# Kernel tuning notes

Measured on AMD Instinct MI355X. Metric: run time of the kernel, lower is better.

## Reference

```python
import jax, jax.numpy as jnp
import numpy as np

C = 180; NH = 6; WS = 8; SS = 4; MLP_RATIO = 2
HD = C // NH
SCALE = HD ** (-0.5)
N = WS * WS  # tokens per window


def _rel_pos_index():
    coords = np.stack(np.meshgrid(np.arange(WS), np.arange(WS), indexing='ij'))  # (2,WS,WS)
    flat = coords.reshape(2, -1)  # (2, N)
    rel = (flat[:, :, None] - flat[:, None, :]).transpose(1, 2, 0)  # (N,N,2)
    rel = rel + np.array([WS - 1, WS - 1])
    rel[:, :, 0] *= 2 * WS - 1
    return rel.sum(-1)  # (N,N) int


def _shift_mask(H, W):
    img_mask = np.zeros((H, W), dtype=np.float32)
    slices = (slice(0, -WS), slice(-WS, -SS), slice(-SS, None))
    cnt = 0
    for hs in slices:
        for ws_ in slices:
            img_mask[hs, ws_] = cnt
            cnt += 1
    mw = img_mask.reshape(H // WS, WS, W // WS, WS).transpose(0, 2, 1, 3).reshape(-1, N)  # (nW, N)
    am = mw[:, None, :] - mw[:, :, None]  # (nW, N, N)
    return np.where(am != 0, np.float32(-100.0), np.float32(0.0))


def _partition(x, H, W):
    # (B,H,W,C) -> (B*nW, N, C)
    B = x.shape[0]
    x = x.reshape(B, H // WS, WS, W // WS, WS, C).transpose(0, 1, 3, 2, 4, 5)
    return x.reshape(-1, N, C)


def _combine(w, B, H, W):
    # (B*nW, N, C) -> (B,H,W,C)
    x = w.reshape(B, H // WS, W // WS, WS, WS, C).transpose(0, 1, 3, 2, 4, 5)
    return x.reshape(B, H, W, C)


def _ln(x, g, b):
    mu = jnp.mean(x, -1, keepdims=True)
    var = jnp.mean(jnp.square(x - mu), -1, keepdims=True)
    return (x - mu) * jax.lax.rsqrt(var + 1e-5) * g + b


def setup_inputs() -> dict:
    key = jax.random.key(0)
    ks = jax.random.split(key, 10)
    B, H, W = 16, 128, 128
    s = 0.02
    return {
        'x': jax.random.normal(ks[0], (B, H * W, C), jnp.float32),
        'ln1_g': jnp.ones((C,), jnp.float32), 'ln1_b': jnp.zeros((C,), jnp.float32),
        'qkv_w': jax.random.normal(ks[1], (3 * C, C), jnp.float32) * s,
        'qkv_b': jnp.zeros((3 * C,), jnp.float32),
        'proj_w': jax.random.normal(ks[2], (C, C), jnp.float32) * s,
        'proj_b': jnp.zeros((C,), jnp.float32),
        'rpb_table': jax.random.normal(ks[3], ((2 * WS - 1) ** 2, NH), jnp.float32) * s,
        'ln2_g': jnp.ones((C,), jnp.float32), 'ln2_b': jnp.zeros((C,), jnp.float32),
        'fc1_w': jax.random.normal(ks[4], (MLP_RATIO * C, C), jnp.float32) * s,
        'fc1_b': jnp.zeros((MLP_RATIO * C,), jnp.float32),
        'fc2_w': jax.random.normal(ks[5], (C, MLP_RATIO * C), jnp.float32) * s,
        'fc2_b': jnp.zeros((C,), jnp.float32),
        'img_height': 128, 'img_width': 128,
    }


def reference(x, ln1_g, ln1_b, qkv_w, qkv_b, proj_w, proj_b, rpb_table,
              ln2_g, ln2_b, fc1_w, fc1_b, fc2_w, fc2_b, img_height, img_width):
    H, W = int(img_height), int(img_width)
    B = x.shape[0]
    rpi = jnp.asarray(_rel_pos_index().reshape(-1))           # (N*N,) static
    mask = jnp.asarray(_shift_mask(H, W))                     # (nW, N, N) static
    nW = (H // WS) * (W // WS)

    residual = x
    h = _ln(x, ln1_g, ln1_b).reshape(B, H, W, C)
    h = jnp.roll(h, (-SS, -SS), axis=(1, 2))
    xw = _partition(h, H, W)                                  # (B*nW, N, C)

    qkv = xw @ qkv_w.T + qkv_b                                # (B*nW, N, 3C)
    qkv = qkv.reshape(-1, N, 3, NH, HD).transpose(2, 0, 3, 1, 4)
    q, k, v = qkv[0] * SCALE, qkv[1], qkv[2]                  # (B*nW, NH, N, HD)
    scores = jnp.einsum('whnd,whmd->whnm', q, k)              # (B*nW, NH, N, N)
    bias = rpb_table[rpi].reshape(N, N, NH).transpose(2, 0, 1)  # (NH,N,N)
    scores = scores + bias[None]
    scores = scores.reshape(B, nW, NH, N, N) + mask[None, :, None]
    probs = jax.nn.softmax(scores.reshape(-1, NH, N, N), axis=-1)
    out = jnp.einsum('whnm,whmd->whnd', probs, v)             # (B*nW, NH, N, HD)
    out = out.transpose(0, 2, 1, 3).reshape(-1, N, C)
    out = out @ proj_w.T + proj_b

    h = _combine(out, B, H, W)
    h = jnp.roll(h, (SS, SS), axis=(1, 2)).reshape(B, H * W, C)
    h = h + residual
    m = _ln(h, ln2_g, ln2_b)
    m = jax.nn.gelu(m @ fc1_w.T + fc1_b, approximate=False) @ fc2_w.T + fc2_b
    return h + m
```

## Files before the change

kernel.cpp:

```cpp
#include <hip/hip_runtime.h>
#include <hip/hip_bf16.h>

typedef short s16x8 __attribute__((ext_vector_type(8)));
typedef short s16x4 __attribute__((ext_vector_type(4)));
typedef float f32x4 __attribute__((ext_vector_type(4)));

__device__ __forceinline__ short f2bf(float f) {
    __bf16 h = (__bf16)f;
    return __builtin_bit_cast(short, h);
}
__device__ __forceinline__ float bf2f(short s) {
    return __builtin_bit_cast(float, ((unsigned int)(unsigned short)s) << 16);
}
__device__ __forceinline__ unsigned int pk2(float a, float b) {
    return (unsigned int)(unsigned short)f2bf(a) | ((unsigned int)(unsigned short)f2bf(b) << 16);
}
__device__ __forceinline__ float plo(unsigned int u) { return bf2f((short)(u & 0xFFFFu)); }
__device__ __forceinline__ float phi(unsigned int u) { return bf2f((short)(u >> 16)); }
__device__ __forceinline__ f32x4 mfma16(s16x8 a, s16x8 b, f32x4 c) {
    return __builtin_amdgcn_mfma_f32_16x16x32_bf16(a, b, c, 0, 0, 0);
}
__device__ __forceinline__ s16x8 ld_b64x2(const short* p) {
    union { s16x8 v; s16x4 h[2]; } u;
    u.h[0] = *(const s16x4*)p;
    u.h[1] = *(const s16x4*)(p + 4);
    return u.v;
}
__device__ __forceinline__ s16x4 pack4(f32x4 a) {
    s16x4 w;
    w[0] = f2bf(a[0]); w[1] = f2bf(a[1]); w[2] = f2bf(a[2]); w[3] = f2bf(a[3]);
    return w;
}

#define SCALE_Q 0.18257418583505536f
#define ONE_BF16 ((short)0x3F80)
#define RA 204
#define PS 76
#define HS 108


__global__ void k_prep(const float* __restrict__ qkv_w, const float* __restrict__ qkv_b,
                       const float* __restrict__ proj_w, const float* __restrict__ proj_b,
                       const float* __restrict__ fc1_w, const float* __restrict__ fc1_b,
                       const float* __restrict__ fc2_w,
                       const float* __restrict__ rpb,
                       short* __restrict__ Whead, short* __restrict__ Wproj,
                       short* __restrict__ Wfc1, short* __restrict__ Wfc2,
                       short* __restrict__ battn) {
    int gt = blockIdx.x * 256 + threadIdx.x;
    int stride = gridDim.x * 256;
    for (int idx = gt; idx < 6 * 96 * 192; idx += stride) {
        int h = idx / (96 * 192), rem = idx - h * 96 * 192;
        int rr = rem / 192, kk = rem - rr * 192;
        int seg = rr >> 5, hd = rr & 31;
        float val = 0.f;
        if (hd < 30) {
            int ch = seg * 180 + h * 30 + hd;
            if (kk < 180) val = qkv_w[ch * 180 + kk];
            else if (kk == 180) val = qkv_b[ch];
            if (seg == 0) val *= SCALE_Q;
        }
        Whead[idx] = f2bf(val);
    }
    for (int idx = gt; idx < 192 * 192; idx += stride) {
        int rr = idx / 192, kk = idx - rr * 192;
        float val = 0.f;
        if (rr < 180) {
            if (kk < 180) val = proj_w[rr * 180 + kk];
            else if (kk == 180) val = proj_b[rr];
        }
        Wproj[idx] = f2bf(val);
    }
    for (int idx = gt; idx < 384 * 192; idx += stride) {
        int rr = idx / 192, kk = idx - rr * 192;
        float val = 0.f;
        if (rr < 360) {
            if (kk < 180) val = fc1_w[rr * 180 + kk];
            else if (kk == 180) val = fc1_b[rr];
        }
        Wfc1[idx] = f2bf(val);
    }
    for (int idx = gt; idx < 192 * 384; idx += stride) {
        int rr = idx / 384, kk = idx - rr * 384;
        Wfc2[idx] = (rr < 180 && kk < 360) ? f2bf(fc2_w[rr * 360 + kk]) : (short)0;
    }
    for (int idx = gt; idx < 6 * 64 * 64; idx += stride) {
        int h = idx >> 12, n = (idx >> 6) & 63, m = idx & 63;
        int r1 = n >> 3, c1 = n & 7, r2 = m >> 3, c2 = m & 7;
        int ridx = (r1 - r2 + 7) * 15 + (c1 - c2 + 7);
        battn[idx] = f2bf(rpb[ridx * 6 + h]);
    }
}

__global__ __launch_bounds__(768, 3)
void k_fused(const float* __restrict__ x, const float* __restrict__ g1, const float* __restrict__ b1,
             const short* __restrict__ Whead,
             const short* __restrict__ Wproj,
             const short* __restrict__ battn,
             const float* __restrict__ g2, const float* __restrict__ b2,
             const short* __restrict__ Wfc1,
             const short* __restrict__ Wfc2, const float* __restrict__ fb2,
             float* __restrict__ out) {
    __shared__ __align__(16) char smem[138240];

    const int tid = threadIdx.x;
    const int wvg = tid >> 6;
    const int half = (wvg >= 6) ? 1 : 0;
    const int wv = wvg - half * 6;
    const int l = tid & 63, l15 = l & 15, lg = l >> 4;
    const int tl = tid - half * 384;

    char* sm = smem + half * 69120;
    short* xln  = (short*)sm;
    short* xout = (short*)sm;
    short* ylds = (short*)sm;
    short* mo   = (short*)sm;
    short* regP = (short*)(sm + 26112);
    short* pout = regP;
    short* ybuf = regP;
    short* hid  = (short*)(sm + 55296);
    short* patch = regP + wv * 2432;

    const int wid = blockIdx.x * 2 + half;
    const int b = wid >> 8, win = wid & 255, wi = win >> 4, wj = win & 15;
    const bool edge = (wi == 15) || (wj == 15);
    const f32x4 vzero = {0.f, 0.f, 0.f, 0.f};

    const int t = tl >> 2, sub = tl & 3;
    size_t rowbase = 0;
    if (tl < 256) {
        const int r = t >> 3, c = t & 7;
        const int gi = (wi * 8 + r + 4) & 127, gj = (wj * 8 + c + 4) & 127;
        rowbase = ((size_t)b * 16384 + (size_t)gi * 128 + gj) * 180;
    }
    const float* xrow = x + rowbase;
    float* yrow = out + rowbase;

    if (tl < 256) {
        float s1 = 0.f, s2 = 0.f;
        unsigned int pA[12], pB[12];
#pragma unroll
        for (int m = 0; m < 12; ++m) {
            int jj = sub + 4 * m;
            if (jj < 45) {
                float4 t4 = *(const float4*)&xrow[4 * jj];
                s1 += t4.x + t4.y + t4.z + t4.w;
                s2 += t4.x * t4.x + t4.y * t4.y + t4.z * t4.z + t4.w * t4.w;
                pA[m] = pk2(t4.x, t4.y);
                pB[m] = pk2(t4.z, t4.w);
            }
        }
        s1 += __shfl_xor(s1, 1); s2 += __shfl_xor(s2, 1);
        s1 += __shfl_xor(s1, 2); s2 += __shfl_xor(s2, 2);
        const float mu = s1 * (1.f / 180.f);
        const float rstd = rsqrtf(s2 * (1.f / 180.f) - mu * mu + 1e-5f);
#pragma unroll
        for (int m = 0; m < 12; ++m) {
            int jj = sub + 4 * m;
            if (jj < 45) {
                float4 g4 = *(const float4*)&g1[4 * jj];
                float4 b4 = *(const float4*)&b1[4 * jj];
                s16x4 w;
                w[0] = f2bf((plo(pA[m]) - mu) * rstd * g4.x + b4.x);
                w[1] = f2bf((phi(pA[m]) - mu) * rstd * g4.y + b4.y);
                w[2] = f2bf((plo(pB[m]) - mu) * rstd * g4.z + b4.z);
                w[3] = f2bf((phi(pB[m]) - mu) * rstd * g4.w + b4.w);
                *(s16x4*)&xln[t * RA + 4 * jj] = w;
            }
        }
    } else {
        for (int k = tl - 256; k < 64 * 12; k += 128) {
            int rr = k / 12, cc = k - rr * 12;
            xln[rr * RA + 180 + cc] = (cc == 0) ? ONE_BF16 : (short)0;
        }
    }
    __syncthreads();

    const short* Wh = Whead + wv * (96 * 192);
    s16x8 qf[4], kf[4], vf[2][2];

#pragma unroll
    for (int jl = 0; jl < 2; ++jl) {
        f32x4 acc[4] = {vzero, vzero, vzero, vzero};
#pragma unroll
        for (int ks = 0; ks < 6; ++ks) {
            s16x8 bwk = *(const s16x8*)&Wh[(jl * 16 + l15) * 192 + ks * 32 + lg * 8];
#pragma unroll
            for (int i = 0; i < 4; ++i) {
                s16x8 afi = ld_b64x2(&xln[(i * 16 + l15) * RA + ks * 32 + lg * 8]);
                acc[i] = mfma16(bwk, afi, acc[i]);
            }
        }
#pragma unroll
        for (int i = 0; i < 4; ++i)
            *(s16x4*)&patch[(i * 16 + l15) * 36 + jl * 16 + lg * 4] = pack4(acc[i]);
    }
#pragma unroll
    for (int i = 0; i < 4; ++i) qf[i] = ld_b64x2(&patch[(i * 16 + l15) * 36 + lg * 8]);

#pragma unroll
    for (int jl = 0; jl < 2; ++jl) {
        f32x4 acc[4] = {vzero, vzero, vzero, vzero};
#pragma unroll
        for (int ks = 0; ks < 6; ++ks) {
            s16x8 bwk = *(const s16x8*)&Wh[(32 + jl * 16 + l15) * 192 + ks * 32 + lg * 8];
#pragma unroll
            for (int i = 0; i < 4; ++i) {
                s16x8 afi = ld_b64x2(&xln[(i * 16 + l15) * RA + ks * 32 + lg * 8]);
                acc[i] = mfma16(bwk, afi, acc[i]);
            }
        }
#pragma unroll
        for (int i = 0; i < 4; ++i)
            *(s16x4*)&patch[(i * 16 + l15) * 36 + jl * 16 + lg * 4] = pack4(acc[i]);
    }
#pragma unroll
    for (int j = 0; j < 4; ++j) kf[j] = ld_b64x2(&patch[(j * 16 + l15) * 36 + lg * 8]);

#pragma unroll
    for (int jl = 0; jl < 2; ++jl) {
        f32x4 acc[4] = {vzero, vzero, vzero, vzero};
#pragma unroll
        for (int ks = 0; ks < 6; ++ks) {
            s16x8 bwk = *(const s16x8*)&Wh[(64 + jl * 16 + l15) * 192 + ks * 32 + lg * 8];
#pragma unroll
            for (int i = 0; i < 4; ++i) {
                s16x8 afi = ld_b64x2(&xln[(i * 16 + l15) * RA + ks * 32 + lg * 8]);
                acc[i] = mfma16(afi, bwk, acc[i]);
            }
        }
#pragma unroll
        for (int i = 0; i < 4; ++i)
            *(s16x4*)&patch[(jl * 16 + l15) * PS + i * 16 + lg * 4] = pack4(acc[i]);
    }
#pragma unroll
    for (int j2 = 0; j2 < 2; ++j2)
#pragma unroll
        for (int ksv = 0; ksv < 2; ++ksv)
            vf[j2][ksv] = ld_b64x2(&patch[(j2 * 16 + l15) * PS + ksv * 32 + lg * 8]);

    __syncthreads();

    {
        const short* bb = battn + wv * 4096;
#pragma unroll
        for (int i = 0; i < 4; ++i) {
            const int n = i * 16 + l15;
            f32x4 sc[4];
#pragma unroll
            for (int j = 0; j < 4; ++j) sc[j] = mfma16(kf[j], qf[i], vzero);
            int cnt_n = 0;
            if (edge) {
                int rn = n >> 3, cn = n & 7;
                cnt_n = (wi == 15 ? ((rn >= 4) ? 2 : 1) : 0) * 3 + (wj == 15 ? ((cn >= 4) ? 2 : 1) : 0);
            }
            float p[4][4];
#pragma unroll
            for (int j = 0; j < 4; ++j) {
                s16x4 bv = *(const s16x4*)&bb[n * 64 + j * 16 + lg * 4];
#pragma unroll
                for (int tt = 0; tt < 4; ++tt) {
                    float s = sc[j][tt] + bf2f(bv[tt]);
                    if (edge) {
                        int m = j * 16 + lg * 4 + tt;
                        int rm = m >> 3, cm = m & 7;
                        int cnt_m = (wi == 15 ? ((rm >= 4) ? 2 : 1) : 0) * 3 + (wj == 15 ? ((cm >= 4) ? 2 : 1) : 0);
                        if (cnt_m != cnt_n) s -= 100.f;
                    }
                    p[j][tt] = s;
                }
            }
            float m0 = p[0][0];
#pragma unroll
            for (int j = 0; j < 4; ++j)
#pragma unroll
                for (int tt = 0; tt < 4; ++tt) m0 = fmaxf(m0, p[j][tt]);
            m0 = fmaxf(m0, __shfl_xor(m0, 16));
            m0 = fmaxf(m0, __shfl_xor(m0, 32));
            float s0 = 0.f;
#pragma unroll
            for (int j = 0; j < 4; ++j)
#pragma unroll
                for (int tt = 0; tt < 4; ++tt) { float e = __expf(p[j][tt] - m0); p[j][tt] = e; s0 += e; }
            s0 += __shfl_xor(s0, 16);
            s0 += __shfl_xor(s0, 32);
            const float sm0 = __builtin_amdgcn_rcpf(s0);

            short* pb = patch + (i & 1) * 1216;
#pragma unroll
            for (int j = 0; j < 4; ++j) {
                f32x4 ps;
#pragma unroll
                for (int tt = 0; tt < 4; ++tt) ps[tt] = p[j][tt] * sm0;
                *(s16x4*)&pb[l15 * PS + j * 16 + lg * 4] = pack4(ps);
            }
            s16x8 pa0 = ld_b64x2(&pb[l15 * PS + lg * 8]);
            s16x8 pa1 = ld_b64x2(&pb[l15 * PS + 32 + lg * 8]);
            f32x4 ov0 = mfma16(vf[0][0], pa0, vzero);
            ov0 = mfma16(vf[0][1], pa1, ov0);
            f32x4 ov1 = mfma16(vf[1][0], pa0, vzero);
            ov1 = mfma16(vf[1][1], pa1, ov1);
            short* xo = &xout[n * RA + wv * 30];
            unsigned int w0 = pk2(ov0[0], ov0[1]);
            unsigned int w1 = pk2(ov0[2], ov0[3]);
            *(unsigned int*)&xo[lg * 4] = w0;
            *(unsigned int*)&xo[lg * 4 + 2] = w1;
            unsigned int w2 = pk2(ov1[0], ov1[1]);
            if (lg < 3) {
                unsigned int w3 = pk2(ov1[2], ov1[3]);
                *(unsigned int*)&xo[16 + lg * 4] = w2;
                *(unsigned int*)&xo[16 + lg * 4 + 2] = w3;
            } else {
                *(unsigned int*)&xo[28] = w2;
            }
        }
    }
    __syncthreads();

#pragma unroll
    for (int jl = 0; jl < 2; ++jl) {
        const int cb = wv * 32 + jl * 16 + lg * 4;
        f32x4 acc[4] = {vzero, vzero, vzero, vzero};
#pragma unroll
        for (int ks = 0; ks < 6; ++ks) {
            s16x8 bwk = *(const s16x8*)&Wproj[(wv * 32 + jl * 16 + l15) * 192 + ks * 32 + lg * 8];
#pragma unroll
            for (int i = 0; i < 4; ++i) {
                s16x8 afi = ld_b64x2(&xout[(i * 16 + l15) * RA + ks * 32 + lg * 8]);
                acc[i] = mfma16(bwk, afi, acc[i]);
            }
        }
        if (cb <= 176) {
#pragma unroll
            for (int i = 0; i < 4; ++i)
                *(s16x4*)&pout[(i * 16 + l15) * RA + cb] = pack4(acc[i]);
        }
    }
    __syncthreads();

    if (tl < 256) {
        float s1 = 0.f, s2 = 0.f;
        unsigned int pA[12], pB[12];
#pragma unroll
        for (int m = 0; m < 12; ++m) {
            int jj = sub + 4 * m;
            if (jj < 45) {
                float4 x4 = *(const float4*)&xrow[4 * jj];
                s16x4 pv = *(const s16x4*)&pout[t * RA + 4 * jj];
                float4 y4;
                y4.x = x4.x + bf2f(pv[0]); y4.y = x4.y + bf2f(pv[1]);
                y4.z = x4.z + bf2f(pv[2]); y4.w = x4.w + bf2f(pv[3]);
                pA[m] = pk2(y4.x, y4.y);
                pB[m] = pk2(y4.z, y4.w);
                *(unsigned int*)&ybuf[t * RA + 4 * jj] = pA[m];
                *(unsigned int*)&ybuf[t * RA + 4 * jj + 2] = pB[m];
                s1 += y4.x + y4.y + y4.z + y4.w;
                s2 += y4.x * y4.x + y4.y * y4.y + y4.z * y4.z + y4.w * y4.w;
            }
        }
        s1 += __shfl_xor(s1, 1); s2 += __shfl_xor(s2, 1);
        s1 += __shfl_xor(s1, 2); s2 += __shfl_xor(s2, 2);
        const float mu = s1 * (1.f / 180.f);
        const float rstd = rsqrtf(s2 * (1.f / 180.f) - mu * mu + 1e-5f);
#pragma unroll
        for (int m = 0; m < 12; ++m) {
            int jj = sub + 4 * m;
            if (jj < 45) {
                float4 g4 = *(const float4*)&g2[4 * jj];
                float4 b4 = *(const float4*)&b2[4 * jj];
                s16x4 w;
                w[0] = f2bf((plo(pA[m]) - mu) * rstd * g4.x + b4.x);
                w[1] = f2bf((phi(pA[m]) - mu) * rstd * g4.y + b4.y);
                w[2] = f2bf((plo(pB[m]) - mu) * rstd * g4.z + b4.z);
                w[3] = f2bf((phi(pB[m]) - mu) * rstd * g4.w + b4.w);
                *(s16x4*)&ylds[t * RA + 4 * jj] = w;
            }
        }
    } else {
        for (int k = tl - 256; k < 64 * 12; k += 128) {
            int rr = k / 12, cc = k - rr * 12;
            ylds[rr * RA + 180 + cc] = (cc == 0) ? ONE_BF16 : (short)0;
        }
    }
    __syncthreads();

    f32x4 acc3[2][4];
#pragma unroll
    for (int jl = 0; jl < 2; ++jl)
#pragma unroll
        for (int i = 0; i < 4; ++i) acc3[jl][i] = vzero;

#pragma unroll
    for (int q = 0; q < 4; ++q) {
        {
            f32x4 acc[4] = {vzero, vzero, vzero, vzero};
#pragma unroll
            for (int ks = 0; ks < 6; ++ks) {
                s16x8 bwk = *(const s16x8*)&Wfc1[((q * 6 + wv) * 16 + l15) * 192 + ks * 32 + lg * 8];
#pragma unroll
                for (int i = 0; i < 4; ++i) {
                    s16x8 ai = ld_b64x2(&ylds[(i * 16 + l15) * RA + ks * 32 + lg * 8]);
                    acc[i] = mfma16(bwk, ai, acc[i]);
                }
            }
            const int clb = wv * 16 + lg * 4;
#pragma unroll
            for (int i = 0; i < 4; ++i) {
                s16x4 w;
#pragma unroll
                for (int tt = 0; tt < 4; ++tt) {
                    float v = acc[i][tt];
                    float u = v * (1.f + 0.044715f * v * v);
                    float e = __expf(-1.5957691216f * u);
                    w[tt] = f2bf(v * __builtin_amdgcn_rcpf(1.f + e));
                }
                *(s16x4*)&hid[(i * 16 + l15) * HS + clb] = w;
            }
        }
        __syncthreads();
#pragma unroll
        for (int ks = 0; ks < 3; ++ks) {
            s16x8 a[4];
#pragma unroll
            for (int i = 0; i < 4; ++i)
                a[i] = ld_b64x2(&hid[(i * 16 + l15) * HS + ks * 32 + lg * 8]);
#pragma unroll
            for (int jl = 0; jl < 2; ++jl) {
                s16x8 bw2 = *(const s16x8*)&Wfc2[((wv * 2 + jl) * 16 + l15) * 384 + q * 96 + ks * 32 + lg * 8];
#pragma unroll
                for (int i = 0; i < 4; ++i) acc3[jl][i] = mfma16(bw2, a[i], acc3[jl][i]);
            }
        }
        __syncthreads();
    }

#pragma unroll
    for (int jl = 0; jl < 2; ++jl) {
        const int cb = (wv * 2 + jl) * 16 + lg * 4;
        if (cb <= 176) {
            float4 f4 = *(const float4*)&fb2[cb];
#pragma unroll
            for (int i = 0; i < 4; ++i) {
                f32x4 a2;
                a2[0] = acc3[jl][i][0] + f4.x;
                a2[1] = acc3[jl][i][1] + f4.y;
                a2[2] = acc3[jl][i][2] + f4.z;
                a2[3] = acc3[jl][i][3] + f4.w;
                *(s16x4*)&mo[(i * 16 + l15) * RA + cb] = pack4(a2);
            }
        }
    }
    __syncthreads();

    if (tl < 256) {
#pragma unroll
        for (int m = 0; m < 12; ++m) {
            int jj = sub + 4 * m;
            if (jj < 45) {
                s16x4 yv4 = *(const s16x4*)&ybuf[t * RA + 4 * jj];
                s16x4 mv = *(const s16x4*)&mo[t * RA + 4 * jj];
                float4 o;
                o.x = bf2f(yv4[0]) + bf2f(mv[0]);
                o.y = bf2f(yv4[1]) + bf2f(mv[1]);
                o.z = bf2f(yv4[2]) + bf2f(mv[2]);
                o.w = bf2f(yv4[3]) + bf2f(mv[3]);
                *(float4*)&yrow[4 * jj] = o;
            }
        }
    }
}

extern "C" void kernel_launch(void* const* d_in, const int* in_sizes, int n_in,
                              void* d_out, int out_size, void* d_ws, size_t ws_size,
                              hipStream_t stream) {
    (void)in_sizes; (void)n_in; (void)out_size; (void)ws_size;
    const float* x      = (const float*)d_in[0];
    const float* ln1g   = (const float*)d_in[1];
    const float* ln1b   = (const float*)d_in[2];
    const float* qkv_w  = (const float*)d_in[3];
    const float* qkv_b  = (const float*)d_in[4];
    const float* proj_w = (const float*)d_in[5];
    const float* proj_b = (const float*)d_in[6];
    const float* rpb    = (const float*)d_in[7];
    const float* ln2g   = (const float*)d_in[8];
    const float* ln2b   = (const float*)d_in[9];
    const float* fc1_w  = (const float*)d_in[10];
    const float* fc1_b  = (const float*)d_in[11];
    const float* fc2_w  = (const float*)d_in[12];
    const float* fc2_b  = (const float*)d_in[13];
    float* out = (float*)d_out;

    char* ws = (char*)d_ws;
    short* Whead = (short*)(ws + 0);
    short* Wproj = (short*)(ws + 221184);
    short* Wfc1  = (short*)(ws + 294912);
    short* Wfc2  = (short*)(ws + 442368);
    short* battn = (short*)(ws + 589824);

    k_prep<<<256, 256, 0, stream>>>(qkv_w, qkv_b, proj_w, proj_b, fc1_w, fc1_b, fc2_w, rpb,
                                    Whead, Wproj, Wfc1, Wfc2, battn);
    k_fused<<<2048, 768, 0, stream>>>(x, ln1g, ln1b, Whead, Wproj, battn,
                                      ln2g, ln2b, Wfc1, Wfc2, fc2_b, out);
}
```

Before: 488.5 us.

## Double MLP hidden chunk size and keep input rows in registers

```diff
diff --git a/kernel.cpp b/kernel.cpp
--- a/kernel.cpp
+++ b/kernel.cpp
@@ -15,8 +15,6 @@
 __device__ __forceinline__ unsigned int pk2(float a, float b) {
     return (unsigned int)(unsigned short)f2bf(a) | ((unsigned int)(unsigned short)f2bf(b) << 16);
 }
-__device__ __forceinline__ float plo(unsigned int u) { return bf2f((short)(u & 0xFFFFu)); }
-__device__ __forceinline__ float phi(unsigned int u) { return bf2f((short)(u >> 16)); }
 __device__ __forceinline__ f32x4 mfma16(s16x8 a, s16x8 b, f32x4 c) {
     return __builtin_amdgcn_mfma_f32_16x16x32_bf16(a, b, c, 0, 0, 0);
 }
@@ -36,7 +34,7 @@
 #define ONE_BF16 ((short)0x3F80)
 #define RA 204
 #define PS 76
-#define HS 108
+#define HS 196
 
 
 __global__ void k_prep(const float* __restrict__ qkv_w, const float* __restrict__ qkv_b,
@@ -101,7 +99,7 @@
              const short* __restrict__ Wfc1,
              const short* __restrict__ Wfc2, const float* __restrict__ fb2,
              float* __restrict__ out) {
-    __shared__ __align__(16) char smem[138240];
+    __shared__ __align__(16) char smem[160768];
 
     const int tid = threadIdx.x;
     const int wvg = tid >> 6;
@@ -110,7 +108,7 @@
     const int l = tid & 63, l15 = l & 15, lg = l >> 4;
     const int tl = tid - half * 384;
 
-    char* sm = smem + half * 69120;
+    char* sm = smem + half * 80384;
     short* xln  = (short*)sm;
     short* xout = (short*)sm;
     short* ylds = (short*)sm;
@@ -136,18 +134,18 @@
     const float* xrow = x + rowbase;
     float* yrow = out + rowbase;
 
+    float4 xr[12];
+
     if (tl < 256) {
         float s1 = 0.f, s2 = 0.f;
-        unsigned int pA[12], pB[12];
 #pragma unroll
         for (int m = 0; m < 12; ++m) {
             int jj = sub + 4 * m;
             if (jj < 45) {
                 float4 t4 = *(const float4*)&xrow[4 * jj];
+                xr[m] = t4;
                 s1 += t4.x + t4.y + t4.z + t4.w;
                 s2 += t4.x * t4.x + t4.y * t4.y + t4.z * t4.z + t4.w * t4.w;
-                pA[m] = pk2(t4.x, t4.y);
-                pB[m] = pk2(t4.z, t4.w);
             }
         }
         s1 += __shfl_xor(s1, 1); s2 += __shfl_xor(s2, 1);
@@ -161,10 +159,10 @@
                 float4 g4 = *(const float4*)&g1[4 * jj];
                 float4 b4 = *(const float4*)&b1[4 * jj];
                 s16x4 w;
-                w[0] = f2bf((plo(pA[m]) - mu) * rstd * g4.x + b4.x);
-                w[1] = f2bf((phi(pA[m]) - mu) * rstd * g4.y + b4.y);
-                w[2] = f2bf((plo(pB[m]) - mu) * rstd * g4.z + b4.z);
-                w[3] = f2bf((phi(pB[m]) - mu) * rstd * g4.w + b4.w);
+                w[0] = f2bf((xr[m].x - mu) * rstd * g4.x + b4.x);
+                w[1] = f2bf((xr[m].y - mu) * rstd * g4.y + b4.y);
+                w[2] = f2bf((xr[m].z - mu) * rstd * g4.z + b4.z);
+                w[3] = f2bf((xr[m].w - mu) * rstd * g4.w + b4.w);
                 *(s16x4*)&xln[t * RA + 4 * jj] = w;
             }
         }
@@ -345,11 +343,10 @@
         for (int m = 0; m < 12; ++m) {
             int jj = sub + 4 * m;
             if (jj < 45) {
-                float4 x4 = *(const float4*)&xrow[4 * jj];
                 s16x4 pv = *(const s16x4*)&pout[t * RA + 4 * jj];
                 float4 y4;
-                y4.x = x4.x + bf2f(pv[0]); y4.y = x4.y + bf2f(pv[1]);
-                y4.z = x4.z + bf2f(pv[2]); y4.w = x4.w + bf2f(pv[3]);
+                y4.x = xr[m].x + bf2f(pv[0]); y4.y = xr[m].y + bf2f(pv[1]);
+                y4.z = xr[m].z + bf2f(pv[2]); y4.w = xr[m].w + bf2f(pv[3]);
                 pA[m] = pk2(y4.x, y4.y);
                 pB[m] = pk2(y4.z, y4.w);
                 *(unsigned int*)&ybuf[t * RA + 4 * jj] = pA[m];
@@ -368,11 +365,15 @@
             if (jj < 45) {
                 float4 g4 = *(const float4*)&g2[4 * jj];
                 float4 b4 = *(const float4*)&b2[4 * jj];
+                float ylo0 = bf2f((short)(pA[m] & 0xFFFFu));
+                float yhi0 = bf2f((short)(pA[m] >> 16));
+                float ylo1 = bf2f((short)(pB[m] & 0xFFFFu));
+                float yhi1 = bf2f((short)(pB[m] >> 16));
                 s16x4 w;
-                w[0] = f2bf((plo(pA[m]) - mu) * rstd * g4.x + b4.x);
-                w[1] = f2bf((phi(pA[m]) - mu) * rstd * g4.y + b4.y);
-                w[2] = f2bf((plo(pB[m]) - mu) * rstd * g4.z + b4.z);
-                w[3] = f2bf((phi(pB[m]) - mu) * rstd * g4.w + b4.w);
+                w[0] = f2bf((ylo0 - mu) * rstd * g4.x + b4.x);
+                w[1] = f2bf((yhi0 - mu) * rstd * g4.y + b4.y);
+                w[2] = f2bf((ylo1 - mu) * rstd * g4.z + b4.z);
+                w[3] = f2bf((yhi1 - mu) * rstd * g4.w + b4.w);
                 *(s16x4*)&ylds[t * RA + 4 * jj] = w;
             }
         }
@@ -391,19 +392,20 @@
         for (int i = 0; i < 4; ++i) acc3[jl][i] = vzero;
 
 #pragma unroll
-    for (int q = 0; q < 4; ++q) {
-        {
+    for (int kh = 0; kh < 2; ++kh) {
+#pragma unroll
+        for (int jl = 0; jl < 2; ++jl) {
             f32x4 acc[4] = {vzero, vzero, vzero, vzero};
 #pragma unroll
             for (int ks = 0; ks < 6; ++ks) {
-                s16x8 bwk = *(const s16x8*)&Wfc1[((q * 6 + wv) * 16 + l15) * 192 + ks * 32 + lg * 8];
+                s16x8 bwk = *(const s16x8*)&Wfc1[((kh * 12 + wv * 2 + jl) * 16 + l15) * 192 + ks * 32 + lg * 8];
 #pragma unroll
                 for (int i = 0; i < 4; ++i) {
                     s16x8 ai = ld_b64x2(&ylds[(i * 16 + l15) * RA + ks * 32 + lg * 8]);
                     acc[i] = mfma16(bwk, ai, acc[i]);
                 }
             }
-            const int clb = wv * 16 + lg * 4;
+            const int clb = (wv * 2 + jl) * 16 + lg * 4;
 #pragma unroll
             for (int i = 0; i < 4; ++i) {
                 s16x4 w;
@@ -419,14 +421,14 @@
         }
         __syncthreads();
 #pragma unroll
-        for (int ks = 0; ks < 3; ++ks) {
+        for (int ks = 0; ks < 6; ++ks) {
             s16x8 a[4];
 #pragma unroll
             for (int i = 0; i < 4; ++i)
                 a[i] = ld_b64x2(&hid[(i * 16 + l15) * HS + ks * 32 + lg * 8]);
 #pragma unroll
             for (int jl = 0; jl < 2; ++jl) {
-                s16x8 bw2 = *(const s16x8*)&Wfc2[((wv * 2 + jl) * 16 + l15) * 384 + q * 96 + ks * 32 + lg * 8];
+                s16x8 bw2 = *(const s16x8*)&Wfc2[((wv * 2 + jl) * 16 + l15) * 384 + kh * 192 + ks * 32 + lg * 8];
 #pragma unroll
                 for (int i = 0; i < 4; ++i) acc3[jl][i] = mfma16(bw2, a[i], acc3[jl][i]);
             }
```

Result: faster. 467.7 us, median of 3 (-4.3%).
